# Kernel tuning notes

Hardware: AMD Instinct MI355X
Metric: run time of the kernel (lower is better)

## Reference

```python
import jax, jax.numpy as jnp
import numpy as np
import math

GROUPS = 32
EPS = 1e-5
N_HEADS = 8  # channels=512 / num_head_channels=64


def group_norm(x, w, b):
    # x: [B, C, T]; GroupNorm over (channels-in-group, T)
    B, C, T = x.shape
    xg = x.reshape(B, GROUPS, C // GROUPS * T)
    mu = xg.mean(axis=-1, keepdims=True)
    var = xg.var(axis=-1, keepdims=True)
    xn = ((xg - mu) * jax.lax.rsqrt(var + EPS)).reshape(B, C, T)
    return xn * w[None, :, None] + b[None, :, None]


def setup_inputs() -> dict:
    key = jax.random.key(0)
    ks = jax.random.split(key, 7)
    C = 512
    return {
        "x": jax.random.normal(ks[0], (8, C, 32, 32), dtype=jnp.float32),
        "norm_w": jax.random.normal(ks[1], (C,), dtype=jnp.float32),
        "norm_b": jax.random.normal(ks[2], (C,), dtype=jnp.float32),
        "qkv_w": jax.random.normal(ks[3], (3 * C, C), dtype=jnp.float32) * 0.02,
        "qkv_b": jax.random.normal(ks[4], (3 * C,), dtype=jnp.float32) * 0.02,
        "proj_w": jax.random.normal(ks[5], (C, C), dtype=jnp.float32) * 0.02,
        "proj_b": jax.random.normal(ks[6], (C,), dtype=jnp.float32) * 0.02,
    }


def reference(x, norm_w, norm_b, qkv_w, qkv_b, proj_w, proj_b):
    b, c, H, W = x.shape
    T = H * W
    xf = x.reshape(b, c, T)
    xn = group_norm(xf, norm_w, norm_b)
    # 1x1 conv1d == channel matmul: [3C, C] x [B, C, T] -> [B, 3C, T]
    qkv = jnp.einsum('oc,bct->bot', qkv_w, xn) + qkv_b[None, :, None]
    ch = c // N_HEADS
    qkv = qkv.reshape(b * N_HEADS, 3 * ch, T)
    q, k, v = qkv[:, :ch], qkv[:, ch:2 * ch], qkv[:, 2 * ch:]
    scale = 1.0 / math.sqrt(math.sqrt(ch))
    # [BH, T, T] score matrix (explicit, as in the original)
    weight = jnp.einsum('bct,bcs->bts', q * scale, k * scale)
    weight = jax.nn.softmax(weight.astype(jnp.float32), axis=-1).astype(qkv.dtype)
    a = jnp.einsum('bts,bcs->bct', weight, v).reshape(b, c, T)
    hout = jnp.einsum('oc,bct->bot', proj_w, a) + proj_b[None, :, None]
    return (xf + hout).reshape(b, c, H, W)
```

## Files before the change

kernel.cpp:

```cpp
#include <hip/hip_runtime.h>
#include <math.h>

typedef float f32x4_t __attribute__((ext_vector_type(4)));
typedef short bf16x8_t __attribute__((ext_vector_type(8)));

#define B_   8
#define C_   512
#define T_   1024
#define NH_  8
#define CH_  64
#define EPSF 1e-5f

#define MFMA16(a, b, c) __builtin_amdgcn_mfma_f32_16x16x32_bf16((a), (b), (c), 0, 0, 0)

#define GLD16(gp, lp) __builtin_amdgcn_global_load_lds( \
    (const __attribute__((address_space(1))) unsigned int*)(gp), \
    (__attribute__((address_space(3))) unsigned int*)(lp), 16, 0, 0)

__device__ __forceinline__ unsigned short f2bf(float f) {
  union { float f; unsigned u; } v; v.f = f;
  unsigned r = v.u + 0x7FFFu + ((v.u >> 16) & 1u);
  return (unsigned short)(r >> 16);
}

__global__ __launch_bounds__(256) void prep_gn_kernel(
    const float* __restrict__ x, const float* __restrict__ w,
    const float* __restrict__ bvec, unsigned short* __restrict__ xnT,
    const float* __restrict__ qw_f, const float* __restrict__ pw_f,
    unsigned short* __restrict__ qw, unsigned short* __restrict__ pw)
{
  int tid = threadIdx.x;
  if (blockIdx.x >= 256) {
    int idx = (blockIdx.x - 256) * 256 + tid;
    const int N1 = 1536 * 512 / 4;
    const int N2 = 512 * 512 / 4;
    if (idx < N1) {
      float4 v = ((const float4*)qw_f)[idx];
      uint2 o;
      o.x = (unsigned)f2bf(v.x) | ((unsigned)f2bf(v.y) << 16);
      o.y = (unsigned)f2bf(v.z) | ((unsigned)f2bf(v.w) << 16);
      ((uint2*)qw)[idx] = o;
    } else if (idx < N1 + N2) {
      int j = idx - N1;
      float4 v = ((const float4*)pw_f)[j];
      uint2 o;
      o.x = (unsigned)f2bf(v.x) | ((unsigned)f2bf(v.y) << 16);
      o.y = (unsigned)f2bf(v.z) | ((unsigned)f2bf(v.w) << 16);
      ((uint2*)pw)[j] = o;
    }
    return;
  }

  int blk = blockIdx.x;
  int b = blk >> 5, g = blk & 31;
  const float* xp = x + ((size_t)(b * C_ + g * 16)) * T_;
  const int N = 16 * T_;

  float s = 0.f, s2 = 0.f;
  for (int i = tid * 4; i < N; i += 256 * 4) {
    float4 v = *(const float4*)(xp + i);
    s  += v.x + v.y + v.z + v.w;
    s2 += v.x * v.x + v.y * v.y + v.z * v.z + v.w * v.w;
  }
  for (int off = 32; off; off >>= 1) {
    s  += __shfl_down(s,  off, 64);
    s2 += __shfl_down(s2, off, 64);
  }
  __shared__ float rs_[4], r2_[4];
  __shared__ float mu_s, rsig_s;
  int wid = tid >> 6, lane = tid & 63;
  if (lane == 0) { rs_[wid] = s; r2_[wid] = s2; }
  __syncthreads();
  if (tid == 0) {
    float ts = rs_[0] + rs_[1] + rs_[2] + rs_[3];
    float t2 = r2_[0] + r2_[1] + r2_[2] + r2_[3];
    float mu = ts / (float)N;
    float var = t2 / (float)N - mu * mu;
    mu_s = mu;
    rsig_s = rsqrtf(var + EPSF);
  }
  __syncthreads();
  float mu = mu_s, rs = rsig_s;

  float wl[16], bl[16];
  for (int c = 0; c < 16; ++c) { wl[c] = w[g * 16 + c]; bl[c] = bvec[g * 16 + c]; }

  for (int t = tid; t < T_; t += 256) {
    unsigned short buf[16] __attribute__((aligned(16)));
    for (int c = 0; c < 16; ++c) {
      float val = xp[(size_t)c * T_ + t];
      buf[c] = f2bf((val - mu) * rs * wl[c] + bl[c]);
    }
    unsigned short* dst = xnT + ((size_t)b * T_ + t) * C_ + g * 16;
    *(uint4*)dst       = *(uint4*)buf;
    *(uint4*)(dst + 8) = *(uint4*)(buf + 8);
  }
}

__global__ __launch_bounds__(256) void gemm_qkv_kernel(
    const unsigned short* __restrict__ W, const unsigned short* __restrict__ xnT,
    const float* __restrict__ bias,
    unsigned short* __restrict__ q_t, unsigned short* __restrict__ k_t,
    unsigned short* __restrict__ v_c)
{
  int b = blockIdx.z;
  int m0 = blockIdx.y * 128, n0 = blockIdx.x * 128;
  int tid = threadIdx.x;
  int w = tid >> 6, lane = tid & 63, quad = lane >> 4, lr = lane & 15;
  int wm = w >> 1, wn = w & 1;

  __shared__ __align__(16) unsigned short Asl[2][128][32];
  __shared__ __align__(16) unsigned short Bsl[2][128][32];

  f32x4_t acc[4][4];
  for (int i = 0; i < 4; ++i)
    for (int j = 0; j < 4; ++j) acc[i][j] = (f32x4_t){0.f, 0.f, 0.f, 0.f};

  int ur = tid >> 2, uk = (tid & 3) * 8;
  const unsigned short* Ap = W + (size_t)(m0 + ur) * C_ + uk;
  const unsigned short* Bp = xnT + ((size_t)b * T_ + n0 + ur) * C_ + uk;

#define STAGE_QKV(buf, k0)                                        \
  do {                                                            \
    GLD16(Ap + (k0),            &Asl[buf][w * 16][0]);            \
    GLD16(Ap + 64 * C_ + (k0),  &Asl[buf][64 + w * 16][0]);       \
    GLD16(Bp + (k0),            &Bsl[buf][w * 16][0]);            \
    GLD16(Bp + 64 * C_ + (k0),  &Bsl[buf][64 + w * 16][0]);       \
  } while (0)

  STAGE_QKV(0, 0);
  __syncthreads();

  int cur = 0;
  for (int k0 = 0; k0 < C_; k0 += 32) {
    if (k0 + 32 < C_) STAGE_QKV(cur ^ 1, k0 + 32);
    bf16x8_t af[4], bfv[4];
    for (int i = 0; i < 4; ++i) af[i]  = *(bf16x8_t*)&Asl[cur][wm * 64 + i * 16 + lr][quad * 8];
    for (int j = 0; j < 4; ++j) bfv[j] = *(bf16x8_t*)&Bsl[cur][wn * 64 + j * 16 + lr][quad * 8];
    for (int i = 0; i < 4; ++i)
      for (int j = 0; j < 4; ++j)
        acc[i][j] = MFMA16(af[i], bfv[j], acc[i][j]);
    __syncthreads();
    cur ^= 1;
  }
#undef STAGE_QKV

  for (int i = 0; i < 4; ++i) {
    int ob = m0 + wm * 64 + i * 16 + quad * 4;
    int h = ob / 192, r0 = ob % 192;
    for (int j = 0; j < 4; ++j) {
      int t = n0 + wn * 64 + j * 16 + lr;
      if (r0 < 128) {
        unsigned short pk[4] __attribute__((aligned(8)));
      #pragma unroll
        for (int r = 0; r < 4; ++r) pk[r] = f2bf(acc[i][j][r] + bias[ob + r]);
        unsigned short* base = (r0 < 64) ? q_t : k_t;
        int chn = (r0 < 64) ? r0 : r0 - 64;
        *(uint2*)&base[((size_t)(b * NH_ + h) * T_ + t) * CH_ + chn] = *(uint2*)pk;
      } else {
      #pragma unroll
        for (int r = 0; r < 4; ++r) {
          float vv = acc[i][j][r] + bias[ob + r];
          v_c[((size_t)(b * NH_ + h) * CH_ + (r0 - 128 + r)) * T_ + t] = f2bf(vv);
        }
      }
    }
  }
}

__global__ __launch_bounds__(256) void attn_kernel(
    const unsigned short* __restrict__ q_t, const unsigned short* __restrict__ k_t,
    const unsigned short* __restrict__ v_c, unsigned short* __restrict__ a_t)
{
  int bh = blockIdx.x;
  int t0 = blockIdx.y * 64;
  int tid = threadIdx.x;
  int w = tid >> 6, lane = tid & 63, quad = lane >> 4, lr = lane & 15;

  __shared__ __align__(16) unsigned short q_s[64][72];
  __shared__ __align__(16) unsigned short k_s[64][72];
  __shared__ __align__(16) unsigned short v_s[64][72];
  __shared__ __align__(16) unsigned short p_s[64][72];

  int r0 = tid >> 3, c0 = (tid & 7) * 8;
  *(uint4*)&q_s[r0][c0] =
      *(const uint4*)&q_t[((size_t)bh * T_ + t0 + r0) * CH_ + c0];
  *(uint4*)&q_s[r0 + 32][c0] =
      *(const uint4*)&q_t[((size_t)bh * T_ + t0 + r0 + 32) * CH_ + c0];

  uint4 kr0 = *(const uint4*)&k_t[((size_t)bh * T_ + r0) * CH_ + c0];
  uint4 kr1 = *(const uint4*)&k_t[((size_t)bh * T_ + r0 + 32) * CH_ + c0];
  uint4 vr0 = *(const uint4*)&v_c[((size_t)bh * CH_ + r0) * T_ + c0];
  uint4 vr1 = *(const uint4*)&v_c[((size_t)bh * CH_ + r0 + 32) * T_ + c0];

  __syncthreads();
  bf16x8_t aq[2];
  aq[0] = *(bf16x8_t*)&q_s[w * 16 + lr][quad * 8];
  aq[1] = *(bf16x8_t*)&q_s[w * 16 + lr][32 + quad * 8];

  bf16x8_t ones8;
  {
    short ov = (lr == 0) ? (short)0x3F80 : (short)0;
    for (int e = 0; e < 8; ++e) ones8[e] = ov;
  }

  f32x4_t o_acc[4], o_l;
  for (int j = 0; j < 4; ++j) o_acc[j] = (f32x4_t){0.f, 0.f, 0.f, 0.f};
  o_l = (f32x4_t){0.f, 0.f, 0.f, 0.f};

  const float SCL = 0.18033688f;
  const float MSH = 11.541560f;

  for (int s0 = 0; s0 < T_; s0 += 64) {
    __syncthreads();
    *(uint4*)&k_s[r0][c0]      = kr0;
    *(uint4*)&k_s[r0 + 32][c0] = kr1;
    *(uint4*)&v_s[r0][c0]      = vr0;
    *(uint4*)&v_s[r0 + 32][c0] = vr1;
    if (s0 + 64 < T_) {
      kr0 = *(const uint4*)&k_t[((size_t)bh * T_ + s0 + 64 + r0) * CH_ + c0];
      kr1 = *(const uint4*)&k_t[((size_t)bh * T_ + s0 + 96 + r0) * CH_ + c0];
      vr0 = *(const uint4*)&v_c[((size_t)bh * CH_ + r0) * T_ + s0 + 64 + c0];
      vr1 = *(const uint4*)&v_c[((size_t)bh * CH_ + r0 + 32) * T_ + s0 + 64 + c0];
    }
    __syncthreads();

    f32x4_t sc[4];
    for (int j = 0; j < 4; ++j) {
      f32x4_t a2 = (f32x4_t){0.f, 0.f, 0.f, 0.f};
      for (int kk = 0; kk < 2; ++kk) {
        bf16x8_t bk = *(bf16x8_t*)&k_s[j * 16 + lr][kk * 32 + quad * 8];
        a2 = MFMA16(aq[kk], bk, a2);
      }
      sc[j] = a2;
    }

    for (int j = 0; j < 4; ++j)
      for (int r = 0; r < 4; ++r) {
        float p = __builtin_amdgcn_exp2f(sc[j][r] * SCL - MSH);
        union { float f; unsigned u; } cv; cv.f = p;
        p_s[w * 16 + quad * 4 + r][j * 16 + lr] = (unsigned short)(cv.u >> 16);
      }
    bf16x8_t ap[2];
    ap[0] = *(bf16x8_t*)&p_s[w * 16 + lr][quad * 8];
    ap[1] = *(bf16x8_t*)&p_s[w * 16 + lr][32 + quad * 8];

    o_l = MFMA16(ap[0], ones8, o_l);
    o_l = MFMA16(ap[1], ones8, o_l);
    for (int j = 0; j < 4; ++j)
      for (int kk = 0; kk < 2; ++kk) {
        bf16x8_t bv = *(bf16x8_t*)&v_s[j * 16 + lr][kk * 32 + quad * 8];
        o_acc[j] = MFMA16(ap[kk], bv, o_acc[j]);
      }
  }

  float lv[4];
  for (int r = 0; r < 4; ++r) lv[r] = __shfl(o_l[r], lane & 48, 64);
  for (int r = 0; r < 4; ++r) {
    float inv = 1.f / lv[r];
    for (int j = 0; j < 4; ++j)
      q_s[w * 16 + quad * 4 + r][j * 16 + lr] = f2bf(o_acc[j][r] * inv);
  }
  __syncthreads();
  *(uint4*)&a_t[((size_t)bh * T_ + t0 + r0) * CH_ + c0]      = *(uint4*)&q_s[r0][c0];
  *(uint4*)&a_t[((size_t)bh * T_ + t0 + r0 + 32) * CH_ + c0] = *(uint4*)&q_s[r0 + 32][c0];
}

__global__ __launch_bounds__(256) void gemm_proj_kernel(
    const unsigned short* __restrict__ W, const unsigned short* __restrict__ a_t,
    const float* __restrict__ bias, const float* __restrict__ xres,
    float* __restrict__ out)
{
  int b = blockIdx.z;
  int m0 = blockIdx.y * 128, n0 = blockIdx.x * 128;
  int tid = threadIdx.x;
  int w = tid >> 6, lane = tid & 63, quad = lane >> 4, lr = lane & 15;
  int wm = w >> 1, wn = w & 1;

  __shared__ __align__(16) unsigned short Asl[2][128][32];
  __shared__ __align__(16) unsigned short Bsl[2][128][32];

  f32x4_t acc[4][4];
  for (int i = 0; i < 4; ++i)
    for (int j = 0; j < 4; ++j) acc[i][j] = (f32x4_t){0.f, 0.f, 0.f, 0.f};

  int ur = tid >> 2, uk = (tid & 3) * 8;
  const unsigned short* Ap = W + (size_t)(m0 + ur) * C_ + uk;

#define STAGE_PROJ(buf, k0)                                                   \
  do {                                                                        \
    const unsigned short* Bp = a_t +                                          \
        ((size_t)(b * NH_ + ((k0) >> 6)) * T_ + n0 + ur) * CH_ + ((k0) & 63) + uk; \
    GLD16(Ap + (k0),           &Asl[buf][w * 16][0]);                         \
    GLD16(Ap + 64 * C_ + (k0), &Asl[buf][64 + w * 16][0]);                    \
    GLD16(Bp,                  &Bsl[buf][w * 16][0]);                         \
    GLD16(Bp + 64 * CH_,       &Bsl[buf][64 + w * 16][0]);                    \
  } while (0)

  STAGE_PROJ(0, 0);
  __syncthreads();

  int cur = 0;
  for (int k0 = 0; k0 < C_; k0 += 32) {
    if (k0 + 32 < C_) STAGE_PROJ(cur ^ 1, k0 + 32);
    bf16x8_t af[4], bfv[4];
    for (int i = 0; i < 4; ++i) af[i]  = *(bf16x8_t*)&Asl[cur][wm * 64 + i * 16 + lr][quad * 8];
    for (int j = 0; j < 4; ++j) bfv[j] = *(bf16x8_t*)&Bsl[cur][wn * 64 + j * 16 + lr][quad * 8];
    for (int i = 0; i < 4; ++i)
      for (int j = 0; j < 4; ++j)
        acc[i][j] = MFMA16(af[i], bfv[j], acc[i][j]);
    __syncthreads();
    cur ^= 1;
  }
#undef STAGE_PROJ

  for (int i = 0; i < 4; ++i) {
    int ob = m0 + wm * 64 + i * 16 + quad * 4;
    for (int j = 0; j < 4; ++j) {
      int t = n0 + wn * 64 + j * 16 + lr;
    #pragma unroll
      for (int r = 0; r < 4; ++r) {
        size_t idx = ((size_t)(b * C_ + ob + r)) * T_ + t;
        out[idx] = acc[i][j][r] + bias[ob + r] + xres[idx];
      }
    }
  }
}

extern "C" void kernel_launch(void* const* d_in, const int* in_sizes, int n_in,
                              void* d_out, int out_size, void* d_ws, size_t ws_size,
                              hipStream_t stream)
{
  const float* x      = (const float*)d_in[0];
  const float* norm_w = (const float*)d_in[1];
  const float* norm_b = (const float*)d_in[2];
  const float* qkv_w  = (const float*)d_in[3];
  const float* qkv_b  = (const float*)d_in[4];
  const float* proj_w = (const float*)d_in[5];
  const float* proj_b = (const float*)d_in[6];
  float* out = (float*)d_out;

  char* ws = (char*)d_ws;
  unsigned short* qw  = (unsigned short*)ws;
  unsigned short* pw  = (unsigned short*)(ws + 1572864);
  unsigned short* xnT = (unsigned short*)(ws + 2097152);
  unsigned short* q_t = (unsigned short*)(ws + 10485760);
  unsigned short* k_t = (unsigned short*)(ws + 18874368);
  unsigned short* v_c = (unsigned short*)(ws + 27262976);
  unsigned short* a_t = (unsigned short*)(ws + 35651584);

  prep_gn_kernel<<<dim3(256 + 1024), dim3(256), 0, stream>>>(
      x, norm_w, norm_b, xnT, qkv_w, proj_w, qw, pw);

  gemm_qkv_kernel<<<dim3(T_ / 128, 1536 / 128, B_), dim3(256), 0, stream>>>(
      qw, xnT, qkv_b, q_t, k_t, v_c);

  attn_kernel<<<dim3(B_ * NH_, T_ / 64), dim3(256), 0, stream>>>(q_t, k_t, v_c, a_t);

  gemm_proj_kernel<<<dim3(T_ / 128, C_ / 128, B_), dim3(256), 0, stream>>>(
      pw, a_t, proj_b, x, out);
}
```

Measured before the change: 168.7 us.

## Process 128 query rows per attention block to reuse K/V tiles

Each attention workgroup now covers 128 query rows instead of 64, with each wave handling two 16-row blocks so every K and V fragment read from shared memory feeds two MFMAs. This halves the number of blocks and the total K/V global and LDS traffic per query, and interleaves independent MFMA chains. MFMA sections are also wrapped in s_setprio to favor matrix issue. The cost is more registers and LDS per block and a grid of 512 blocks, which may lower occupancy and parallelism on the large GPU.

New measurement: 164.1 us. 1.03x faster.

```diff
diff --git a/kernel.cpp b/kernel.cpp
--- a/kernel.cpp
+++ b/kernel.cpp
@@ -173,20 +173,20 @@
     const unsigned short* __restrict__ v_c, unsigned short* __restrict__ a_t)
 {
   int bh = blockIdx.x;
-  int t0 = blockIdx.y * 64;
+  int t0 = blockIdx.y * 128;
   int tid = threadIdx.x;
   int w = tid >> 6, lane = tid & 63, quad = lane >> 4, lr = lane & 15;
 
-  __shared__ __align__(16) unsigned short q_s[64][72];
+  __shared__ __align__(16) unsigned short q_s[128][72];
+  __shared__ __align__(16) unsigned short p_s[128][72];
   __shared__ __align__(16) unsigned short k_s[64][72];
   __shared__ __align__(16) unsigned short v_s[64][72];
-  __shared__ __align__(16) unsigned short p_s[64][72];
 
   int r0 = tid >> 3, c0 = (tid & 7) * 8;
-  *(uint4*)&q_s[r0][c0] =
-      *(const uint4*)&q_t[((size_t)bh * T_ + t0 + r0) * CH_ + c0];
-  *(uint4*)&q_s[r0 + 32][c0] =
-      *(const uint4*)&q_t[((size_t)bh * T_ + t0 + r0 + 32) * CH_ + c0];
+#pragma unroll
+  for (int cch = 0; cch < 4; ++cch)
+    *(uint4*)&q_s[r0 + 32 * cch][c0] =
+        *(const uint4*)&q_t[((size_t)bh * T_ + t0 + r0 + 32 * cch) * CH_ + c0];
 
   uint4 kr0 = *(const uint4*)&k_t[((size_t)bh * T_ + r0) * CH_ + c0];
   uint4 kr1 = *(const uint4*)&k_t[((size_t)bh * T_ + r0 + 32) * CH_ + c0];
@@ -194,9 +194,12 @@
   uint4 vr1 = *(const uint4*)&v_c[((size_t)bh * CH_ + r0 + 32) * T_ + c0];
 
   __syncthreads();
-  bf16x8_t aq[2];
-  aq[0] = *(bf16x8_t*)&q_s[w * 16 + lr][quad * 8];
-  aq[1] = *(bf16x8_t*)&q_s[w * 16 + lr][32 + quad * 8];
+  bf16x8_t aq[2][2];
+#pragma unroll
+  for (int rb = 0; rb < 2; ++rb) {
+    aq[rb][0] = *(bf16x8_t*)&q_s[w * 32 + rb * 16 + lr][quad * 8];
+    aq[rb][1] = *(bf16x8_t*)&q_s[w * 32 + rb * 16 + lr][32 + quad * 8];
+  }
 
   bf16x8_t ones8;
   {
@@ -204,9 +207,12 @@
     for (int e = 0; e < 8; ++e) ones8[e] = ov;
   }
 
-  f32x4_t o_acc[4], o_l;
-  for (int j = 0; j < 4; ++j) o_acc[j] = (f32x4_t){0.f, 0.f, 0.f, 0.f};
-  o_l = (f32x4_t){0.f, 0.f, 0.f, 0.f};
+  f32x4_t o_acc[2][4], o_l[2];
+#pragma unroll
+  for (int rb = 0; rb < 2; ++rb) {
+    for (int j = 0; j < 4; ++j) o_acc[rb][j] = (f32x4_t){0.f, 0.f, 0.f, 0.f};
+    o_l[rb] = (f32x4_t){0.f, 0.f, 0.f, 0.f};
+  }
 
   const float SCL = 0.18033688f;
   const float MSH = 11.541560f;
@@ -225,45 +231,75 @@
     }
     __syncthreads();
 
-    f32x4_t sc[4];
+    f32x4_t sc[2][4];
+    __builtin_amdgcn_s_setprio(1);
+#pragma unroll
     for (int j = 0; j < 4; ++j) {
-      f32x4_t a2 = (f32x4_t){0.f, 0.f, 0.f, 0.f};
+      f32x4_t a0 = (f32x4_t){0.f, 0.f, 0.f, 0.f};
+      f32x4_t a1 = (f32x4_t){0.f, 0.f, 0.f, 0.f};
+#pragma unroll
       for (int kk = 0; kk < 2; ++kk) {
         bf16x8_t bk = *(bf16x8_t*)&k_s[j * 16 + lr][kk * 32 + quad * 8];
-        a2 = MFMA16(aq[kk], bk, a2);
+        a0 = MFMA16(aq[0][kk], bk, a0);
+        a1 = MFMA16(aq[1][kk], bk, a1);
       }
-      sc[j] = a2;
-    }
-
+      sc[0][j] = a0;
+      sc[1][j] = a1;
+    }
+    __builtin_amdgcn_s_setprio(0);
+
+#pragma unroll
+    for (int rb = 0; rb < 2; ++rb)
+#pragma unroll
+      for (int j = 0; j < 4; ++j)
+#pragma unroll
+        for (int r = 0; r < 4; ++r) {
+          float p = __builtin_amdgcn_exp2f(sc[rb][j][r] * SCL - MSH);
+          union { float f; unsigned u; } cv; cv.f = p;
+          p_s[w * 32 + rb * 16 + quad * 4 + r][j * 16 + lr] = (unsigned short)(cv.u >> 16);
+        }
+    bf16x8_t ap[2][2];
+#pragma unroll
+    for (int rb = 0; rb < 2; ++rb) {
+      ap[rb][0] = *(bf16x8_t*)&p_s[w * 32 + rb * 16 + lr][quad * 8];
+      ap[rb][1] = *(bf16x8_t*)&p_s[w * 32 + rb * 16 + lr][32 + quad * 8];
+    }
+
+    __builtin_amdgcn_s_setprio(1);
+#pragma unroll
+    for (int rb = 0; rb < 2; ++rb) {
+      o_l[rb] = MFMA16(ap[rb][0], ones8, o_l[rb]);
+      o_l[rb] = MFMA16(ap[rb][1], ones8, o_l[rb]);
+    }
+#pragma unroll
     for (int j = 0; j < 4; ++j)
-      for (int r = 0; r < 4; ++r) {
-        float p = __builtin_amdgcn_exp2f(sc[j][r] * SCL - MSH);
-        union { float f; unsigned u; } cv; cv.f = p;
-        p_s[w * 16 + quad * 4 + r][j * 16 + lr] = (unsigned short)(cv.u >> 16);
-      }
-    bf16x8_t ap[2];
-    ap[0] = *(bf16x8_t*)&p_s[w * 16 + lr][quad * 8];
-    ap[1] = *(bf16x8_t*)&p_s[w * 16 + lr][32 + quad * 8];
-
-    o_l = MFMA16(ap[0], ones8, o_l);
-    o_l = MFMA16(ap[1], ones8, o_l);
-    for (int j = 0; j < 4; ++j)
+#pragma unroll
       for (int kk = 0; kk < 2; ++kk) {
         bf16x8_t bv = *(bf16x8_t*)&v_s[j * 16 + lr][kk * 32 + quad * 8];
-        o_acc[j] = MFMA16(ap[kk], bv, o_acc[j]);
+        o_acc[0][j] = MFMA16(ap[0][kk], bv, o_acc[0][j]);
+        o_acc[1][j] = MFMA16(ap[1][kk], bv, o_acc[1][j]);
       }
-  }
-
-  float lv[4];
-  for (int r = 0; r < 4; ++r) lv[r] = __shfl(o_l[r], lane & 48, 64);
-  for (int r = 0; r < 4; ++r) {
-    float inv = 1.f / lv[r];
-    for (int j = 0; j < 4; ++j)
-      q_s[w * 16 + quad * 4 + r][j * 16 + lr] = f2bf(o_acc[j][r] * inv);
-  }
-  __syncthreads();
-  *(uint4*)&a_t[((size_t)bh * T_ + t0 + r0) * CH_ + c0]      = *(uint4*)&q_s[r0][c0];
-  *(uint4*)&a_t[((size_t)bh * T_ + t0 + r0 + 32) * CH_ + c0] = *(uint4*)&q_s[r0 + 32][c0];
+    __builtin_amdgcn_s_setprio(0);
+  }
+
+#pragma unroll
+  for (int rb = 0; rb < 2; ++rb) {
+    float lv[4];
+#pragma unroll
+    for (int r = 0; r < 4; ++r) lv[r] = __shfl(o_l[rb][r], lane & 48, 64);
+#pragma unroll
+    for (int r = 0; r < 4; ++r) {
+      float inv = 1.f / lv[r];
+#pragma unroll
+      for (int j = 0; j < 4; ++j)
+        q_s[w * 32 + rb * 16 + quad * 4 + r][j * 16 + lr] = f2bf(o_acc[rb][j][r] * inv);
+    }
+  }
+  __syncthreads();
+#pragma unroll
+  for (int cch = 0; cch < 4; ++cch)
+    *(uint4*)&a_t[((size_t)bh * T_ + t0 + r0 + 32 * cch) * CH_ + c0] =
+        *(uint4*)&q_s[r0 + 32 * cch][c0];
 }
 
 __global__ __launch_bounds__(256) void gemm_proj_kernel(
@@ -355,7 +391,7 @@
   gemm_qkv_kernel<<<dim3(T_ / 128, 1536 / 128, B_), dim3(256), 0, stream>>>(
       qw, xnT, qkv_b, q_t, k_t, v_c);
 
-  attn_kernel<<<dim3(B_ * NH_, T_ / 64), dim3(256), 0, stream>>>(q_t, k_t, v_c, a_t);
+  attn_kernel<<<dim3(B_ * NH_, T_ / 128), dim3(256), 0, stream>>>(q_t, k_t, v_c, a_t);
 
   gemm_proj_kernel<<<dim3(T_ / 128, C_ / 128, B_), dim3(256), 0, stream>>>(
       pw, a_t, proj_b, x, out);
```
